# Optimization experiments

Hardware: AMD Instinct MI355X
Metric: run time of the kernel (lower is better)

## Reference

```python
import jax, jax.numpy as jnp
import numpy as np

B, L, C = 16, 2048, 128
FACTOR = 5
EPS = 1e-5


def setup_inputs() -> dict:
    key = jax.random.key(0)
    ks = jax.random.split(key, 16)
    U = min(FACTOR * int(np.ceil(np.log(L))), L)  # U_part == u == 40 for L=2048
    inp = {"x": jax.random.normal(ks[0], (B, L, C), jnp.float32)}
    scalar_names = ["Wq", "bq", "Wk", "bk", "Wv", "bv", "Wo", "bo", "w1", "b1", "w2", "b2"]
    for i, n in enumerate(scalar_names):
        inp[n] = jax.random.normal(ks[i + 1], (1,), jnp.float32) * 0.5
    inp["g1"] = jnp.ones((1,), jnp.float32)
    inp["beta1"] = jnp.zeros((1,), jnp.float32)
    inp["g2"] = jnp.ones((1,), jnp.float32)
    inp["beta2"] = jnp.zeros((1,), jnp.float32)
    # ProbAttention's random key-sampling indices (torch.randint(L_K, (L_Q, sample_k)))
    inp["index_sample"] = jax.random.randint(ks[14], (L, U), 0, L, dtype=jnp.int32)
    return inp


def _layernorm(x, g, b):
    # norm_dims=2 with d_model=1: normalize jointly over (seq_len, 1) == seq axis here
    m = x.mean(-1, keepdims=True)
    v = x.var(-1, keepdims=True)
    return (x - m) * jax.lax.rsqrt(v + EPS) * g + b


def reference(x, Wq, bq, Wk, bk, Wv, bv, Wo, bo, w1, b1, w2, b2,
              g1, beta1, g2, beta2, index_sample):
    U = index_sample.shape[1]  # sample_k == n_top (L_Q == L_K)
    batch_idx = jnp.arange(B)[:, None]

    def chan(xc):  # xc: [B, L] one channel, d_model=1 squeezed (H=1, D=1 -> scale=1)
        q = xc * Wq + bq
        k = xc * Wk + bk
        v = xc * Wv + bv
        # sparse measurement: sample U keys per query
        K_s = k[:, index_sample]                      # [B, L, U]
        QK = q[:, :, None] * K_s                      # [B, L, U]
        M = QK.max(-1) - QK.sum(-1) / L               # [B, L]
        _, M_top = jax.lax.top_k(M, U)                # [B, U] top-u query indices
        Qr = jnp.take_along_axis(q, M_top, axis=1)    # [B, U]
        scores = Qr[:, :, None] * k[:, None, :]       # [B, U, L], scale = 1/sqrt(1)
        attn = jax.nn.softmax(scores, axis=-1)
        upd = jnp.einsum('bul,bl->bu', attn, v)       # [B, U]
        # initial context = mean of V (mask_flag=False), updated at top queries
        ctx = jnp.broadcast_to(v.mean(1, keepdims=True), xc.shape)
        ctx = ctx.at[batch_idx, M_top].set(upd)       # [B, L]
        new_x = ctx * Wo + bo                          # out_projection
        x1 = _layernorm(xc + new_x, g1, beta1)
        y = jax.nn.gelu(x1 * w1 + b1, approximate=False)  # conv1 (1x1, 1->1) + gelu
        y = y * w2 + b2                                    # conv2 (1x1, 1->1)
        return _layernorm(x1 + y, g2, beta2)

    # all cfg.d_model encoder layers share one weight set -> vmap over channels
    return jax.vmap(chan, in_axes=2, out_axes=2)(x)  # [B, L, C]
```

## Files before the change

### kernel.cpp

```cpp
#include <hip/hip_runtime.h>
#include <math.h>

#define LL 2048
#define CC 128
#define BB 16
#define UU 40
#define NT 256
#define NW 4
#define EPSF 1e-5f

__device__ __forceinline__ float waveSum(float v) {
#pragma unroll
    for (int off = 1; off < 64; off <<= 1) v += __shfl_xor(v, off, 64);
    return v;
}
__device__ __forceinline__ float waveMax(float v) {
#pragma unroll
    for (int off = 1; off < 64; off <<= 1) v = fmaxf(v, __shfl_xor(v, off, 64));
    return v;
}
__device__ __forceinline__ float waveMin(float v) {
#pragma unroll
    for (int off = 1; off < 64; off <<= 1) v = fminf(v, __shfl_xor(v, off, 64));
    return v;
}
__device__ __forceinline__ float blockSum(float v, volatile float* scr) {
    v = waveSum(v);
    const int lane = threadIdx.x & 63, wid = threadIdx.x >> 6;
    __syncthreads();
    if (lane == 0) scr[wid] = v;
    __syncthreads();
    return scr[0] + scr[1] + scr[2] + scr[3];
}

__global__ __launch_bounds__(256) void transpose_dual(
    const float* __restrict__ x,  float* __restrict__ xT,
    const float* __restrict__ M,  float* __restrict__ MT) {
    __shared__ float t[32][33];
    const int z  = blockIdx.z;
    const int b  = (z < BB) ? z : (z - BB);
    const float* in  = (z < BB) ? x  : M;
    float* outp      = (z < BB) ? xT : MT;
    const int c0 = blockIdx.x * 32, l0 = blockIdx.y * 32;
    const int lx = threadIdx.x, ly = threadIdx.y;
    const float* base = in + ((size_t)b * LL + l0) * CC + c0;
#pragma unroll
    for (int i = 0; i < 4; ++i) t[ly + i * 8][lx] = base[(size_t)(ly + i * 8) * CC + lx];
    __syncthreads();
    float* obase = outp + ((size_t)b * CC + c0) * LL + l0;
#pragma unroll
    for (int i = 0; i < 4; ++i) obase[(size_t)(ly + i * 8) * LL + lx] = t[lx][ly + i * 8];
}
__global__ __launch_bounds__(256) void transpose_out(const float* __restrict__ in,
                                                     float* __restrict__ outp) {
    __shared__ float t[32][33];
    const int b  = blockIdx.z;
    const int l0 = blockIdx.x * 32, c0 = blockIdx.y * 32;
    const int lx = threadIdx.x, ly = threadIdx.y;
    const float* base = in + ((size_t)b * CC + c0) * LL + l0;
#pragma unroll
    for (int i = 0; i < 4; ++i) t[ly + i * 8][lx] = base[(size_t)(ly + i * 8) * LL + lx];
    __syncthreads();
    float* obase = outp + ((size_t)b * LL + l0) * CC + c0;
#pragma unroll
    for (int i = 0; i < 4; ++i) obase[(size_t)(ly + i * 8) * CC + lx] = t[lx][ly + i * 8];
}

__global__ __launch_bounds__(256) void agg_kernel(
    const float* __restrict__ x, const int* __restrict__ idx,
    const float* __restrict__ gWq, const float* __restrict__ gbq,
    const float* __restrict__ gWk, const float* __restrict__ gbk,
    float* __restrict__ M)
{
    __shared__ int s_idx[8 * UU];
    const int tid = threadIdx.x;
    const int g   = blockIdx.x;
    const int b   = ((g & 7) << 1) | ((g >> 3) & 1);
    const int l0  = (g >> 4) * 8;
    if (tid < 256)          s_idx[tid]       = idx[l0 * UU + tid];
    if (tid < 8 * UU - 256) s_idx[256 + tid] = idx[l0 * UU + 256 + tid];
    __syncthreads();

    const int s = tid & 31;
    const int r = tid >> 5;
    const int l = l0 + r;
    const float Wq = *gWq, bq = *gbq, Wk = *gWk, bk = *gbk;

    const float4* xb = (const float4*)(x + (size_t)b * LL * CC);
    float4 xo4 = xb[(size_t)l * 32 + s];
    float xo[4] = {xo4.x, xo4.y, xo4.z, xo4.w};

    float  mx[4] = {-3.4e38f, -3.4e38f, -3.4e38f, -3.4e38f};
    float  mn[4] = { 3.4e38f,  3.4e38f,  3.4e38f,  3.4e38f};
    double sm[4] = {0.0, 0.0, 0.0, 0.0};
    const int* rowp = &s_idx[r * UU];
#pragma unroll 8
    for (int u = 0; u < UU; ++u) {
        const int i = rowp[u];
        float4 xv = xb[(size_t)i * 32 + s];
        float xa[4] = {xv.x, xv.y, xv.z, xv.w};
#pragma unroll
        for (int t = 0; t < 4; ++t) {
            mx[t] = fmaxf(mx[t], xa[t]);
            mn[t] = fminf(mn[t], xa[t]);
            sm[t] += (double)xa[t];
        }
    }
    float mo[4];
#pragma unroll
    for (int t = 0; t < 4; ++t) {
        const float xH = (Wk >= 0.f) ? mx[t] : mn[t];
        const float xL = (Wk >= 0.f) ? mn[t] : mx[t];
        const float kH = __fadd_rn(__fmul_rn(xH, Wk), bk);
        const float kL = __fadd_rn(__fmul_rn(xL, Wk), bk);
        const float q  = __fadd_rn(__fmul_rn(xo[t], Wq), bq);
        const float t1 = __fmul_rn(q, (q >= 0.f) ? kH : kL);
        const double ks = (double)Wk * sm[t] + 40.0 * (double)bk;
        const float t2 = (float)(((double)q * ks) * (1.0 / 2048.0));
        mo[t] = __fsub_rn(t1, t2);
    }
    float4 Mo = make_float4(mo[0], mo[1], mo[2], mo[3]);
    ((float4*)(M + ((size_t)b * LL + l) * CC))[s] = Mo;
}

__global__ __launch_bounds__(NT) void informer_main(
    const float* __restrict__ xT,
    float* MoT,
    const float* __restrict__ gWq, const float* __restrict__ gbq,
    const float* __restrict__ gWk, const float* __restrict__ gbk,
    const float* __restrict__ gWv, const float* __restrict__ gbv,
    const float* __restrict__ gWo, const float* __restrict__ gbo,
    const float* __restrict__ gw1, const float* __restrict__ gb1,
    const float* __restrict__ gw2, const float* __restrict__ gb2,
    const float* __restrict__ gg1, const float* __restrict__ gbe1,
    const float* __restrict__ gg2, const float* __restrict__ gbe2)
{
    const int tid = threadIdx.x;
    const int ln  = tid & 63;
    const int wid = tid >> 6;
    const int blk = blockIdx.x;
    const int b   = blk >> 7;
    const int c   = blk & (CC - 1);

    __shared__ __align__(16) float s_xc[LL];
    __shared__ __align__(16) float s_wk[LL];
    __shared__ float s_red[NW];
    __shared__ float s_cv[NW * UU];
    __shared__ int   s_ci[NW * UU];
    __shared__ int   s_top[UU];
    __shared__ float s_upd[UU];

    const float Wq = *gWq, bq = *gbq, Wk = *gWk, bk = *gbk;
    const float Wv = *gWv, bv = *gbv, Wo = *gWo, bo = *gbo;
    const float w1 = *gw1, b1 = *gb1, w2 = *gw2, b2 = *gb2;
    const float g1 = *gg1, be1 = *gbe1, g2 = *gg2, be2 = *gbe2;

    const float4* xrow4 = (const float4*)(xT + ((size_t)b * CC + c) * LL);
    float* Mrow = MoT + ((size_t)b * CC + c) * LL;
    float4* orow4 = (float4*)Mrow;
    float4* s_xc4 = (float4*)s_xc;
    float4* s_wk4 = (float4*)s_wk;

    float4 kv[8], vv[8];
    float vsum = 0.f, kmn = 3.4e38f, kmx = -3.4e38f;
#pragma unroll
    for (int m = 0; m < 8; ++m) {
        float4 xv = xrow4[ln + m * 64];
        if (wid == 0) s_xc4[ln + m * 64] = xv;
        float4 kk, vx;
        kk.x = __fadd_rn(__fmul_rn(xv.x, Wk), bk);
        kk.y = __fadd_rn(__fmul_rn(xv.y, Wk), bk);
        kk.z = __fadd_rn(__fmul_rn(xv.z, Wk), bk);
        kk.w = __fadd_rn(__fmul_rn(xv.w, Wk), bk);
        vx.x = __fadd_rn(__fmul_rn(xv.x, Wv), bv);
        vx.y = __fadd_rn(__fmul_rn(xv.y, Wv), bv);
        vx.z = __fadd_rn(__fmul_rn(xv.z, Wv), bv);
        vx.w = __fadd_rn(__fmul_rn(xv.w, Wv), bv);
        kv[m] = kk; vv[m] = vx;
        vsum += vx.x + vx.y + vx.z + vx.w;
        kmx = fmaxf(kmx, fmaxf(fmaxf(kk.x, kk.y), fmaxf(kk.z, kk.w)));
        kmn = fminf(kmn, fminf(fminf(kk.x, kk.y), fminf(kk.z, kk.w)));
    }
    vsum = waveSum(vsum);
    kmx  = waveMax(kmx);
    kmn  = waveMin(kmn);
    const float vmean = vsum * (1.f / (float)LL);

    const int lbase = wid * 512 + ln;
    float mloc[8];
#pragma unroll
    for (int j = 0; j < 8; ++j) mloc[j] = Mrow[lbase + 64 * j];

    float wbv = mloc[0]; int wbi = lbase;
#pragma unroll
    for (int j = 1; j < 8; ++j)
        if (mloc[j] > wbv) { wbv = mloc[j]; wbi = lbase + 64 * j; }

    for (int t = 0; t < UU; ++t) {
        float rv = wbv; int ri = wbi;
#pragma unroll
        for (int off = 1; off < 64; off <<= 1) {
            float ov = __shfl_xor(rv, off, 64);
            int   oi = __shfl_xor(ri, off, 64);
            if (ov > rv || (ov == rv && oi < ri)) { rv = ov; ri = oi; }
        }
        if (ln == 0) { s_cv[wid * UU + t] = rv; s_ci[wid * UU + t] = ri; }
        if (wbi == ri) {
#pragma unroll
            for (int j = 0; j < 8; ++j) if (lbase + 64 * j == ri) mloc[j] = -3.4e38f;
            wbv = mloc[0]; wbi = lbase;
#pragma unroll
            for (int j = 1; j < 8; ++j)
                if (mloc[j] > wbv) { wbv = mloc[j]; wbi = lbase + 64 * j; }
        }
    }
    __syncthreads();

    if (wid == 0) {
        float c0v = s_cv[ln],      c1v = s_cv[ln + 64];
        int   c0i = s_ci[ln],      c1i = s_ci[ln + 64];
        float c2v = (ln < 32) ? s_cv[ln + 128] : -3.4e38f;
        int   c2i = (ln < 32) ? s_ci[ln + 128] : (LL + 1);
        for (int t = 0; t < UU; ++t) {
            float rv = c0v; int ri = c0i;
            if (c1v > rv || (c1v == rv && c1i < ri)) { rv = c1v; ri = c1i; }
            if (c2v > rv || (c2v == rv && c2i < ri)) { rv = c2v; ri = c2i; }
#pragma unroll
            for (int off = 1; off < 64; off <<= 1) {
                float ov = __shfl_xor(rv, off, 64);
                int   oi = __shfl_xor(ri, off, 64);
                if (ov > rv || (ov == rv && oi < ri)) { rv = ov; ri = oi; }
            }
            if (ln == 0) s_top[t] = ri;
            if (c0i == ri) c0v = -3.4e38f;
            else if (c1i == ri) c1v = -3.4e38f;
            else if (c2i == ri) c2v = -3.4e38f;
        }
    }
    __syncthreads();

    for (int r = 0; r < UU / NW; ++r) {
        const int u = r * NW + wid;
        const int p = s_top[u];
        const float qp = __fadd_rn(__fmul_rn(s_xc[p], Wq), bq);
        const float smax = (qp >= 0.f) ? __fmul_rn(qp, kmx) : __fmul_rn(qp, kmn);
        float se = 0.f, sev = 0.f;
#pragma unroll
        for (int m = 0; m < 8; ++m) {
            float4 kk = kv[m], vx = vv[m];
            float e0 = __expf(qp * kk.x - smax);
            float e1 = __expf(qp * kk.y - smax);
            float e2 = __expf(qp * kk.z - smax);
            float e3 = __expf(qp * kk.w - smax);
            se += e0 + e1 + e2 + e3;
            sev = fmaf(e0, vx.x, fmaf(e1, vx.y, fmaf(e2, vx.z, fmaf(e3, vx.w, sev))));
        }
        se  = waveSum(se);
        sev = waveSum(sev);
        if (ln == 0) s_upd[u] = sev / se;
    }
    __syncthreads();

#pragma unroll
    for (int m = 0; m < 2; ++m)
        s_wk4[tid + m * 256] = make_float4(vmean, vmean, vmean, vmean);
    __syncthreads();
    if (tid < UU) s_wk[s_top[tid]] = s_upd[tid];
    __syncthreads();

    float lsum = 0.f;
#pragma unroll
    for (int m = 0; m < 2; ++m) {
        const int f = tid + m * 256;
        float4 cx = s_wk4[f], xc = s_xc4[f], tv;
        tv.x = xc.x + __fadd_rn(__fmul_rn(cx.x, Wo), bo);
        tv.y = xc.y + __fadd_rn(__fmul_rn(cx.y, Wo), bo);
        tv.z = xc.z + __fadd_rn(__fmul_rn(cx.z, Wo), bo);
        tv.w = xc.w + __fadd_rn(__fmul_rn(cx.w, Wo), bo);
        s_wk4[f] = tv;
        lsum += tv.x + tv.y + tv.z + tv.w;
    }
    const float mean1 = blockSum(lsum, s_red) * (1.f / (float)LL);
    float lss = 0.f;
#pragma unroll
    for (int m = 0; m < 2; ++m) {
        float4 tv = s_wk4[tid + m * 256];
        float d0 = tv.x - mean1, d1 = tv.y - mean1, d2 = tv.z - mean1, d3 = tv.w - mean1;
        lss += d0 * d0 + d1 * d1 + d2 * d2 + d3 * d3;
    }
    const float var1 = blockSum(lss, s_red) * (1.f / (float)LL);
    const float rs1 = rsqrtf(var1 + EPSF);

    float lsum2 = 0.f;
#pragma unroll
    for (int m = 0; m < 2; ++m) {
        const int f = tid + m * 256;
        float4 tv = s_wk4[f], zz;
        {
            float x1 = (tv.x - mean1) * rs1 * g1 + be1;
            float a = x1 * w1 + b1;
            float y = 0.5f * a * (1.f + erff(a * 0.70710678118654752f));
            zz.x = x1 + (y * w2 + b2);
        }
        {
            float x1 = (tv.y - mean1) * rs1 * g1 + be1;
            float a = x1 * w1 + b1;
            float y = 0.5f * a * (1.f + erff(a * 0.70710678118654752f));
            zz.y = x1 + (y * w2 + b2);
        }
        {
            float x1 = (tv.z - mean1) * rs1 * g1 + be1;
            float a = x1 * w1 + b1;
            float y = 0.5f * a * (1.f + erff(a * 0.70710678118654752f));
            zz.z = x1 + (y * w2 + b2);
        }
        {
            float x1 = (tv.w - mean1) * rs1 * g1 + be1;
            float a = x1 * w1 + b1;
            float y = 0.5f * a * (1.f + erff(a * 0.70710678118654752f));
            zz.w = x1 + (y * w2 + b2);
        }
        s_wk4[f] = zz;
        lsum2 += zz.x + zz.y + zz.z + zz.w;
    }
    const float mean2 = blockSum(lsum2, s_red) * (1.f / (float)LL);
    float lss2 = 0.f;
#pragma unroll
    for (int m = 0; m < 2; ++m) {
        float4 zz = s_wk4[tid + m * 256];
        float d0 = zz.x - mean2, d1 = zz.y - mean2, d2 = zz.z - mean2, d3 = zz.w - mean2;
        lss2 += d0 * d0 + d1 * d1 + d2 * d2 + d3 * d3;
    }
    const float var2 = blockSum(lss2, s_red) * (1.f / (float)LL);
    const float rs2 = rsqrtf(var2 + EPSF);

#pragma unroll
    for (int m = 0; m < 2; ++m) {
        const int f = tid + m * 256;
        float4 zz = s_wk4[f], oo;
        oo.x = (zz.x - mean2) * rs2 * g2 + be2;
        oo.y = (zz.y - mean2) * rs2 * g2 + be2;
        oo.z = (zz.z - mean2) * rs2 * g2 + be2;
        oo.w = (zz.w - mean2) * rs2 * g2 + be2;
        orow4[f] = oo;
    }
}

__global__ __launch_bounds__(NT) void informer_fallback(
    const float* __restrict__ xin,
    const float* __restrict__ gWq, const float* __restrict__ gbq,
    const float* __restrict__ gWk, const float* __restrict__ gbk,
    const float* __restrict__ gWv, const float* __restrict__ gbv,
    const float* __restrict__ gWo, const float* __restrict__ gbo,
    const float* __restrict__ gw1, const float* __restrict__ gb1,
    const float* __restrict__ gw2, const float* __restrict__ gb2,
    const float* __restrict__ gg1, const float* __restrict__ gbe1,
    const float* __restrict__ gg2, const float* __restrict__ gbe2,
    const int* __restrict__ idx,
    float* __restrict__ outp)
{
    const int tid  = threadIdx.x;
    const int lane = tid & 63;
    const int wid  = tid >> 6;
    const int blk  = blockIdx.x;
    const int b    = blk >> 7;
    const int c    = blk & (CC - 1);

    __shared__ float  s_xc[LL];
    __shared__ float  s_kc[LL];
    __shared__ float  s_v[LL];
    __shared__ float  s_red[NW];
    __shared__ double s_cv[NW * UU];
    __shared__ int    s_ci[NW * UU];
    __shared__ int    s_top[UU];
    __shared__ float  s_upd[UU];

    const float Wq = *gWq, bq = *gbq, Wk = *gWk, bk = *gbk;
    const float Wv = *gWv, bv = *gbv, Wo = *gWo, bo = *gbo;
    const float w1 = *gw1, b1 = *gb1, w2 = *gw2, b2 = *gb2;
    const float g1 = *gg1, be1 = *gbe1, g2 = *gg2, be2 = *gbe2;

    const float* xrow = xin + (size_t)b * LL * CC + c;
    float* orow = outp + (size_t)b * LL * CC + c;

    float vsum = 0.f, kmn = 3.4e38f, kmx = -3.4e38f;
    for (int l = tid; l < LL; l += NT) {
        float xv = xrow[(size_t)l * CC];
        s_xc[l] = xv;
        float kvv = __fadd_rn(__fmul_rn(xv, Wk), bk);
        float vvv = __fadd_rn(__fmul_rn(xv, Wv), bv);
        s_kc[l] = kvv;
        s_v[l] = vvv;
        vsum += vvv;
        kmn = fminf(kmn, kvv);
        kmx = fmaxf(kmx, kvv);
    }
    const float vmean  = blockSum(vsum, s_red) * (1.f / (float)LL);
    float t1 = waveMax(kmx);
    __syncthreads();
    if (lane == 0) s_red[wid] = t1;
    __syncthreads();
    const float kmxAll = fmaxf(fmaxf(s_red[0], s_red[1]), fmaxf(s_red[2], s_red[3]));
    float t2 = waveMin(kmn);
    __syncthreads();
    if (lane == 0) s_red[wid] = t2;
    __syncthreads();
    const float kmnAll = fminf(fminf(s_red[0], s_red[1]), fminf(s_red[2], s_red[3]));

    double mloc[8];
#pragma unroll
    for (int j = 0; j < 8; ++j) {
        const int l = tid + NT * j;
        const float qv = __fadd_rn(__fmul_rn(s_xc[l], Wq), bq);
        const double qd = (double)qv;
        const int* row = idx + l * UU;
        float kmaxs = -3.4e38f, kmins = 3.4e38f;
        double ssum = 0.0;
#pragma unroll 8
        for (int u = 0; u < UU; ++u) {
            float kvv = s_kc[row[u]];
            kmaxs = fmaxf(kmaxs, kvv);
            kmins = fminf(kmins, kvv);
            ssum += (double)kvv;
        }
        double qmax = (qd >= 0.0) ? qd * (double)kmaxs : qd * (double)kmins;
        mloc[j] = qmax - qd * ssum * (1.0 / (double)LL);
    }

    double wbv = mloc[0]; int wbi = tid;
#pragma unroll
    for (int j = 1; j < 8; ++j)
        if (mloc[j] > wbv) { wbv = mloc[j]; wbi = tid + NT * j; }

    for (int t = 0; t < UU; ++t) {
        double rv = wbv; int ri = wbi;
#pragma unroll
        for (int off = 1; off < 64; off <<= 1) {
            double ov = __shfl_xor(rv, off, 64);
            int    oi = __shfl_xor(ri, off, 64);
            if (ov > rv || (ov == rv && oi < ri)) { rv = ov; ri = oi; }
        }
        if (lane == 0) { s_cv[wid * UU + t] = rv; s_ci[wid * UU + t] = ri; }
        if (wbi == ri) {
#pragma unroll
            for (int j = 0; j < 8; ++j) if ((tid + NT * j) == ri) mloc[j] = -1e300;
            wbv = mloc[0]; wbi = tid;
#pragma unroll
            for (int j = 1; j < 8; ++j)
                if (mloc[j] > wbv) { wbv = mloc[j]; wbi = tid + NT * j; }
        }
    }
    __syncthreads();

    if (wid == 0) {
        double c0v = s_cv[lane], c1v = s_cv[lane + 64];
        int    c0i = s_ci[lane], c1i = s_ci[lane + 64];
        double c2v = (lane < 32) ? s_cv[lane + 128] : -1e300;
        int    c2i = (lane < 32) ? s_ci[lane + 128] : (LL + 1);
        for (int t = 0; t < UU; ++t) {
            double rv = c0v; int ri = c0i;
            if (c1v > rv || (c1v == rv && c1i < ri)) { rv = c1v; ri = c1i; }
            if (c2v > rv || (c2v == rv && c2i < ri)) { rv = c2v; ri = c2i; }
#pragma unroll
            for (int off = 1; off < 64; off <<= 1) {
                double ov = __shfl_xor(rv, off, 64);
                int    oi = __shfl_xor(ri, off, 64);
                if (ov > rv || (ov == rv && oi < ri)) { rv = ov; ri = oi; }
            }
            if (lane == 0) s_top[t] = ri;
            if (c0i == ri) c0v = -1e300;
            else if (c1i == ri) c1v = -1e300;
            else if (c2i == ri) c2v = -1e300;
        }
    }
    __syncthreads();

    for (int r = 0; r < UU / NW; ++r) {
        const int u = r * NW + wid;
        const int p = s_top[u];
        const float qp = __fadd_rn(__fmul_rn(s_xc[p], Wq), bq);
        const float smax = (qp >= 0.f) ? qp * kmxAll : qp * kmnAll;
        float se = 0.f, sev = 0.f;
        for (int l = lane; l < LL; l += 64) {
            float e = __expf(qp * s_kc[l] - smax);
            se += e;
            sev = fmaf(e, s_v[l], sev);
        }
        se = waveSum(se); sev = waveSum(sev);
        if (lane == 0) s_upd[u] = sev / se;
    }
    __syncthreads();

    for (int l = tid; l < LL; l += NT) s_kc[l] = vmean;
    __syncthreads();
    if (tid < UU) s_kc[s_top[tid]] = s_upd[tid];
    __syncthreads();

    float lsum = 0.f;
    for (int l = tid; l < LL; l += NT) {
        float tv = s_xc[l] + __fadd_rn(__fmul_rn(s_kc[l], Wo), bo);
        s_kc[l] = tv;
        lsum += tv;
    }
    const float mean1 = blockSum(lsum, s_red) * (1.f / (float)LL);
    float lss = 0.f;
    for (int l = tid; l < LL; l += NT) { float d = s_kc[l] - mean1; lss += d * d; }
    const float var1 = blockSum(lss, s_red) * (1.f / (float)LL);
    const float rs1 = rsqrtf(var1 + EPSF);

    float lsum2 = 0.f;
    for (int l = tid; l < LL; l += NT) {
        float x1 = (s_kc[l] - mean1) * rs1 * g1 + be1;
        float a  = x1 * w1 + b1;
        float y  = 0.5f * a * (1.f + erff(a * 0.70710678118654752f));
        y = y * w2 + b2;
        float z = x1 + y;
        s_kc[l] = z;
        lsum2 += z;
    }
    const float mean2 = blockSum(lsum2, s_red) * (1.f / (float)LL);
    float lss2 = 0.f;
    for (int l = tid; l < LL; l += NT) { float d = s_kc[l] - mean2; lss2 += d * d; }
    const float var2 = blockSum(lss2, s_red) * (1.f / (float)LL);
    const float rs2 = rsqrtf(var2 + EPSF);

    for (int l = tid; l < LL; l += NT)
        orow[(size_t)l * CC] = (s_kc[l] - mean2) * rs2 * g2 + be2;
}

extern "C" void kernel_launch(void* const* d_in, const int* in_sizes, int n_in,
                              void* d_out, int out_size, void* d_ws, size_t ws_size,
                              hipStream_t stream) {
    const float* x   = (const float*)d_in[0];
    const float* Wq  = (const float*)d_in[1];
    const float* bq  = (const float*)d_in[2];
    const float* Wk  = (const float*)d_in[3];
    const float* bk  = (const float*)d_in[4];
    const float* Wv  = (const float*)d_in[5];
    const float* bv  = (const float*)d_in[6];
    const float* Wo  = (const float*)d_in[7];
    const float* bo  = (const float*)d_in[8];
    const float* w1  = (const float*)d_in[9];
    const float* b1  = (const float*)d_in[10];
    const float* w2  = (const float*)d_in[11];
    const float* b2  = (const float*)d_in[12];
    const float* g1  = (const float*)d_in[13];
    const float* be1 = (const float*)d_in[14];
    const float* g2  = (const float*)d_in[15];
    const float* be2 = (const float*)d_in[16];
    const int*   idx = (const int*)d_in[17];
    float* out = (float*)d_out;

    const size_t SZ = (size_t)BB * LL * CC * sizeof(float);

    if (ws_size >= 2 * SZ) {
        float* xT = (float*)d_ws;
        float* MT = (float*)((char*)d_ws + SZ);
        agg_kernel<<<dim3((LL / 8) * BB), dim3(256), 0, stream>>>(x, idx, Wq, bq, Wk, bk, out);
        transpose_dual<<<dim3(CC / 32, LL / 32, 2 * BB), dim3(32, 8), 0, stream>>>(x, xT, out, MT);
        informer_main<<<dim3(BB * CC), dim3(NT), 0, stream>>>(
            xT, MT, Wq, bq, Wk, bk, Wv, bv, Wo, bo, w1, b1, w2, b2,
            g1, be1, g2, be2);
        transpose_out<<<dim3(LL / 32, CC / 32, BB), dim3(32, 8), 0, stream>>>(MT, out);
    } else {
        informer_fallback<<<dim3(BB * CC), dim3(NT), 0, stream>>>(
            x, Wq, bq, Wk, bk, Wv, bv, Wo, bo, w1, b1, w2, b2,
            g1, be1, g2, be2, idx, out);
    }
}
```

Before: 292.8 us.

## Process one (batch,channel) row per wavefront instead of per block

The main kernel now gives each wavefront its own (b,c) row, with 4 rows per block, where before a whole 256-thread block handled one row. This removes the block-level syncthreads reductions and the two-stage cross-wave top-k merge, since top-40 selection, softmax updates and both layernorms now use only wave shuffles. The softmax pass handles 4 top queries at once and recomputes k from x in registers, and the k max/min come from the x max/min. In exchange each thread holds many more registers (8 float4 of M, x and temporaries), which may lower occupancy. The serial 40-step top-k loop is also now done by one wave over 2048 elements instead of being split across 4 waves.

```diff
diff --git a/kernel.cpp b/kernel.cpp
--- a/kernel.cpp
+++ b/kernel.cpp
@@ -31,6 +31,22 @@
     if (lane == 0) scr[wid] = v;
     __syncthreads();
     return scr[0] + scr[1] + scr[2] + scr[3];
+}
+__device__ __forceinline__ float blockMax(float v, volatile float* scr) {
+    v = waveMax(v);
+    const int lane = threadIdx.x & 63, wid = threadIdx.x >> 6;
+    __syncthreads();
+    if (lane == 0) scr[wid] = v;
+    __syncthreads();
+    return fmaxf(fmaxf(scr[0], scr[1]), fmaxf(scr[2], scr[3]));
+}
+__device__ __forceinline__ float blockMin(float v, volatile float* scr) {
+    v = waveMin(v);
+    const int lane = threadIdx.x & 63, wid = threadIdx.x >> 6;
+    __syncthreads();
+    if (lane == 0) scr[wid] = v;
+    __syncthreads();
+    return fminf(fminf(scr[0], scr[1]), fminf(scr[2], scr[3]));
 }
 
 __global__ __launch_bounds__(256) void transpose_dual(
@@ -123,7 +139,7 @@
     ((float4*)(M + ((size_t)b * LL + l) * CC))[s] = Mo;
 }
 
-__global__ __launch_bounds__(NT) void informer_main(
+__global__ __launch_bounds__(NT) void rowBC(
     const float* __restrict__ xT,
     float* MoT,
     const float* __restrict__ gWq, const float* __restrict__ gbq,
@@ -138,164 +154,152 @@
     const int tid = threadIdx.x;
     const int ln  = tid & 63;
     const int wid = tid >> 6;
-    const int blk = blockIdx.x;
-    const int b   = blk >> 7;
-    const int c   = blk & (CC - 1);
-
-    __shared__ __align__(16) float s_xc[LL];
-    __shared__ __align__(16) float s_wk[LL];
-    __shared__ float s_red[NW];
-    __shared__ float s_cv[NW * UU];
-    __shared__ int   s_ci[NW * UU];
-    __shared__ int   s_top[UU];
-    __shared__ float s_upd[UU];
+    const int r   = blockIdx.x * 4 + wid;
+
+    __shared__ __align__(16) float s_ctx[4][LL];
+    __shared__ int s_top[4][UU];
 
     const float Wq = *gWq, bq = *gbq, Wk = *gWk, bk = *gbk;
     const float Wv = *gWv, bv = *gbv, Wo = *gWo, bo = *gbo;
     const float w1 = *gw1, b1 = *gb1, w2 = *gw2, b2 = *gb2;
     const float g1 = *gg1, be1 = *gbe1, g2 = *gg2, be2 = *gbe2;
 
-    const float4* xrow4 = (const float4*)(xT + ((size_t)b * CC + c) * LL);
-    float* Mrow = MoT + ((size_t)b * CC + c) * LL;
+    const float*  xrow  = xT + (size_t)r * LL;
+    const float4* xrow4 = (const float4*)xrow;
+    float* Mrow = MoT + (size_t)r * LL;
+    const float4* mrow4 = (const float4*)Mrow;
     float4* orow4 = (float4*)Mrow;
-    float4* s_xc4 = (float4*)s_xc;
-    float4* s_wk4 = (float4*)s_wk;
-
-    float4 kv[8], vv[8];
-    float vsum = 0.f, kmn = 3.4e38f, kmx = -3.4e38f;
-#pragma unroll
-    for (int m = 0; m < 8; ++m) {
-        float4 xv = xrow4[ln + m * 64];
-        if (wid == 0) s_xc4[ln + m * 64] = xv;
-        float4 kk, vx;
-        kk.x = __fadd_rn(__fmul_rn(xv.x, Wk), bk);
-        kk.y = __fadd_rn(__fmul_rn(xv.y, Wk), bk);
-        kk.z = __fadd_rn(__fmul_rn(xv.z, Wk), bk);
-        kk.w = __fadd_rn(__fmul_rn(xv.w, Wk), bk);
-        vx.x = __fadd_rn(__fmul_rn(xv.x, Wv), bv);
-        vx.y = __fadd_rn(__fmul_rn(xv.y, Wv), bv);
-        vx.z = __fadd_rn(__fmul_rn(xv.z, Wv), bv);
-        vx.w = __fadd_rn(__fmul_rn(xv.w, Wv), bv);
-        kv[m] = kk; vv[m] = vx;
-        vsum += vx.x + vx.y + vx.z + vx.w;
-        kmx = fmaxf(kmx, fmaxf(fmaxf(kk.x, kk.y), fmaxf(kk.z, kk.w)));
-        kmn = fminf(kmn, fminf(fminf(kk.x, kk.y), fminf(kk.z, kk.w)));
-    }
-    vsum = waveSum(vsum);
-    kmx  = waveMax(kmx);
-    kmn  = waveMin(kmn);
-    const float vmean = vsum * (1.f / (float)LL);
-
-    const int lbase = wid * 512 + ln;
-    float mloc[8];
-#pragma unroll
-    for (int j = 0; j < 8; ++j) mloc[j] = Mrow[lbase + 64 * j];
-
-    float wbv = mloc[0]; int wbi = lbase;
-#pragma unroll
-    for (int j = 1; j < 8; ++j)
-        if (mloc[j] > wbv) { wbv = mloc[j]; wbi = lbase + 64 * j; }
-
+    float4* lds4  = (float4*)s_ctx[wid];
+
+    float4 mv[8];
+#pragma unroll
+    for (int m = 0; m < 8; ++m) mv[m] = mrow4[ln + m * 64];
+
+    float bvv = -3.4e38f; int bii = LL + 1;
+#pragma unroll
+    for (int m = 0; m < 8; ++m) {
+        const int l0 = 4 * (ln + 64 * m);
+        if (mv[m].x > bvv) { bvv = mv[m].x; bii = l0; }
+        if (mv[m].y > bvv) { bvv = mv[m].y; bii = l0 + 1; }
+        if (mv[m].z > bvv) { bvv = mv[m].z; bii = l0 + 2; }
+        if (mv[m].w > bvv) { bvv = mv[m].w; bii = l0 + 3; }
+    }
     for (int t = 0; t < UU; ++t) {
-        float rv = wbv; int ri = wbi;
+        float rv = bvv; int ri = bii;
 #pragma unroll
         for (int off = 1; off < 64; off <<= 1) {
             float ov = __shfl_xor(rv, off, 64);
             int   oi = __shfl_xor(ri, off, 64);
             if (ov > rv || (ov == rv && oi < ri)) { rv = ov; ri = oi; }
         }
-        if (ln == 0) { s_cv[wid * UU + t] = rv; s_ci[wid * UU + t] = ri; }
-        if (wbi == ri) {
-#pragma unroll
-            for (int j = 0; j < 8; ++j) if (lbase + 64 * j == ri) mloc[j] = -3.4e38f;
-            wbv = mloc[0]; wbi = lbase;
-#pragma unroll
-            for (int j = 1; j < 8; ++j)
-                if (mloc[j] > wbv) { wbv = mloc[j]; wbi = lbase + 64 * j; }
-        }
-    }
-    __syncthreads();
-
-    if (wid == 0) {
-        float c0v = s_cv[ln],      c1v = s_cv[ln + 64];
-        int   c0i = s_ci[ln],      c1i = s_ci[ln + 64];
-        float c2v = (ln < 32) ? s_cv[ln + 128] : -3.4e38f;
-        int   c2i = (ln < 32) ? s_ci[ln + 128] : (LL + 1);
-        for (int t = 0; t < UU; ++t) {
-            float rv = c0v; int ri = c0i;
-            if (c1v > rv || (c1v == rv && c1i < ri)) { rv = c1v; ri = c1i; }
-            if (c2v > rv || (c2v == rv && c2i < ri)) { rv = c2v; ri = c2i; }
-#pragma unroll
-            for (int off = 1; off < 64; off <<= 1) {
-                float ov = __shfl_xor(rv, off, 64);
-                int   oi = __shfl_xor(ri, off, 64);
-                if (ov > rv || (ov == rv && oi < ri)) { rv = ov; ri = oi; }
+        if (ln == 0) s_top[wid][t] = ri;
+        if (bii == ri) {
+#pragma unroll
+            for (int m = 0; m < 8; ++m) {
+                const int l0 = 4 * (ln + 64 * m);
+                if (l0     == ri) mv[m].x = -3.4e38f;
+                if (l0 + 1 == ri) mv[m].y = -3.4e38f;
+                if (l0 + 2 == ri) mv[m].z = -3.4e38f;
+                if (l0 + 3 == ri) mv[m].w = -3.4e38f;
             }
-            if (ln == 0) s_top[t] = ri;
-            if (c0i == ri) c0v = -3.4e38f;
-            else if (c1i == ri) c1v = -3.4e38f;
-            else if (c2i == ri) c2v = -3.4e38f;
-        }
-    }
-    __syncthreads();
-
-    for (int r = 0; r < UU / NW; ++r) {
-        const int u = r * NW + wid;
-        const int p = s_top[u];
-        const float qp = __fadd_rn(__fmul_rn(s_xc[p], Wq), bq);
-        const float smax = (qp >= 0.f) ? __fmul_rn(qp, kmx) : __fmul_rn(qp, kmn);
-        float se = 0.f, sev = 0.f;
+            bvv = -3.4e38f; bii = LL + 1;
+#pragma unroll
+            for (int m = 0; m < 8; ++m) {
+                const int l0 = 4 * (ln + 64 * m);
+                if (mv[m].x > bvv) { bvv = mv[m].x; bii = l0; }
+                if (mv[m].y > bvv) { bvv = mv[m].y; bii = l0 + 1; }
+                if (mv[m].z > bvv) { bvv = mv[m].z; bii = l0 + 2; }
+                if (mv[m].w > bvv) { bvv = mv[m].w; bii = l0 + 3; }
+            }
+        }
+    }
+
+    float4 xc[8];
+    float vsum = 0.f, xmx = -3.4e38f, xmn = 3.4e38f;
+#pragma unroll
+    for (int m = 0; m < 8; ++m) {
+        float4 xv = xrow4[ln + m * 64];
+        xc[m] = xv;
+        vsum += __fadd_rn(__fmul_rn(xv.x, Wv), bv) + __fadd_rn(__fmul_rn(xv.y, Wv), bv)
+              + __fadd_rn(__fmul_rn(xv.z, Wv), bv) + __fadd_rn(__fmul_rn(xv.w, Wv), bv);
+        xmx = fmaxf(xmx, fmaxf(fmaxf(xv.x, xv.y), fmaxf(xv.z, xv.w)));
+        xmn = fminf(xmn, fminf(fminf(xv.x, xv.y), fminf(xv.z, xv.w)));
+    }
+    vsum = waveSum(vsum);
+    xmx  = waveMax(xmx);
+    xmn  = waveMin(xmn);
+    const float vmean = vsum * (1.f / (float)LL);
+    const float kmx = __fadd_rn(__fmul_rn((Wk >= 0.f) ? xmx : xmn, Wk), bk);
+    const float kmn = __fadd_rn(__fmul_rn((Wk >= 0.f) ? xmn : xmx, Wk), bk);
+
+#pragma unroll
+    for (int m = 0; m < 8; ++m)
+        lds4[ln + m * 64] = make_float4(vmean, vmean, vmean, vmean);
+
+    for (int g = 0; g < UU / 4; ++g) {
+        int p[4]; float qp[4], sm[4];
+#pragma unroll
+        for (int q = 0; q < 4; ++q) {
+            p[q] = s_top[wid][g * 4 + q];
+            const float xq = xrow[p[q]];
+            qp[q] = __fadd_rn(__fmul_rn(xq, Wq), bq);
+            sm[q] = (qp[q] >= 0.f) ? __fmul_rn(qp[q], kmx) : __fmul_rn(qp[q], kmn);
+        }
+        float se[4] = {0.f, 0.f, 0.f, 0.f};
+        float sx[4] = {0.f, 0.f, 0.f, 0.f};
 #pragma unroll
         for (int m = 0; m < 8; ++m) {
-            float4 kk = kv[m], vx = vv[m];
-            float e0 = __expf(qp * kk.x - smax);
-            float e1 = __expf(qp * kk.y - smax);
-            float e2 = __expf(qp * kk.z - smax);
-            float e3 = __expf(qp * kk.w - smax);
-            se += e0 + e1 + e2 + e3;
-            sev = fmaf(e0, vx.x, fmaf(e1, vx.y, fmaf(e2, vx.z, fmaf(e3, vx.w, sev))));
-        }
-        se  = waveSum(se);
-        sev = waveSum(sev);
-        if (ln == 0) s_upd[u] = sev / se;
-    }
-    __syncthreads();
-
-#pragma unroll
-    for (int m = 0; m < 2; ++m)
-        s_wk4[tid + m * 256] = make_float4(vmean, vmean, vmean, vmean);
-    __syncthreads();
-    if (tid < UU) s_wk[s_top[tid]] = s_upd[tid];
-    __syncthreads();
-
+            float4 x4 = xc[m];
+            float4 k4;
+            k4.x = __fadd_rn(__fmul_rn(x4.x, Wk), bk);
+            k4.y = __fadd_rn(__fmul_rn(x4.y, Wk), bk);
+            k4.z = __fadd_rn(__fmul_rn(x4.z, Wk), bk);
+            k4.w = __fadd_rn(__fmul_rn(x4.w, Wk), bk);
+#pragma unroll
+            for (int q = 0; q < 4; ++q) {
+                float e;
+                e = __expf(fmaf(qp[q], k4.x, -sm[q])); se[q] += e; sx[q] = fmaf(e, x4.x, sx[q]);
+                e = __expf(fmaf(qp[q], k4.y, -sm[q])); se[q] += e; sx[q] = fmaf(e, x4.y, sx[q]);
+                e = __expf(fmaf(qp[q], k4.z, -sm[q])); se[q] += e; sx[q] = fmaf(e, x4.z, sx[q]);
+                e = __expf(fmaf(qp[q], k4.w, -sm[q])); se[q] += e; sx[q] = fmaf(e, x4.w, sx[q]);
+            }
+        }
+#pragma unroll
+        for (int q = 0; q < 4; ++q) {
+            const float seA = waveSum(se[q]);
+            const float sxA = waveSum(sx[q]);
+            const float upd = (Wv * sxA + bv * seA) / seA;
+            if (ln == 0) s_ctx[wid][p[q]] = upd;
+        }
+    }
+
+    float4 tt[8];
     float lsum = 0.f;
 #pragma unroll
-    for (int m = 0; m < 2; ++m) {
-        const int f = tid + m * 256;
-        float4 cx = s_wk4[f], xc = s_xc4[f], tv;
-        tv.x = xc.x + __fadd_rn(__fmul_rn(cx.x, Wo), bo);
-        tv.y = xc.y + __fadd_rn(__fmul_rn(cx.y, Wo), bo);
-        tv.z = xc.z + __fadd_rn(__fmul_rn(cx.z, Wo), bo);
-        tv.w = xc.w + __fadd_rn(__fmul_rn(cx.w, Wo), bo);
-        s_wk4[f] = tv;
+    for (int m = 0; m < 8; ++m) {
+        float4 cx = lds4[ln + m * 64], xv = xc[m], tv;
+        tv.x = xv.x + __fadd_rn(__fmul_rn(cx.x, Wo), bo);
+        tv.y = xv.y + __fadd_rn(__fmul_rn(cx.y, Wo), bo);
+        tv.z = xv.z + __fadd_rn(__fmul_rn(cx.z, Wo), bo);
+        tv.w = xv.w + __fadd_rn(__fmul_rn(cx.w, Wo), bo);
+        tt[m] = tv;
         lsum += tv.x + tv.y + tv.z + tv.w;
     }
-    const float mean1 = blockSum(lsum, s_red) * (1.f / (float)LL);
+    const float mean1 = waveSum(lsum) * (1.f / (float)LL);
     float lss = 0.f;
 #pragma unroll
-    for (int m = 0; m < 2; ++m) {
-        float4 tv = s_wk4[tid + m * 256];
+    for (int m = 0; m < 8; ++m) {
+        float4 tv = tt[m];
         float d0 = tv.x - mean1, d1 = tv.y - mean1, d2 = tv.z - mean1, d3 = tv.w - mean1;
         lss += d0 * d0 + d1 * d1 + d2 * d2 + d3 * d3;
     }
-    const float var1 = blockSum(lss, s_red) * (1.f / (float)LL);
+    const float var1 = waveSum(lss) * (1.f / (float)LL);
     const float rs1 = rsqrtf(var1 + EPSF);
 
     float lsum2 = 0.f;
 #pragma unroll
-    for (int m = 0; m < 2; ++m) {
-        const int f = tid + m * 256;
-        float4 tv = s_wk4[f], zz;
+    for (int m = 0; m < 8; ++m) {
+        float4 tv = tt[m], zz;
         {
             float x1 = (tv.x - mean1) * rs1 * g1 + be1;
             float a = x1 * w1 + b1;
@@ -320,29 +324,28 @@
             float y = 0.5f * a * (1.f + erff(a * 0.70710678118654752f));
             zz.w = x1 + (y * w2 + b2);
         }
-        s_wk4[f] = zz;
+        tt[m] = zz;
         lsum2 += zz.x + zz.y + zz.z + zz.w;
     }
-    const float mean2 = blockSum(lsum2, s_red) * (1.f / (float)LL);
+    const float mean2 = waveSum(lsum2) * (1.f / (float)LL);
     float lss2 = 0.f;
 #pragma unroll
-    for (int m = 0; m < 2; ++m) {
-        float4 zz = s_wk4[tid + m * 256];
+    for (int m = 0; m < 8; ++m) {
+        float4 zz = tt[m];
         float d0 = zz.x - mean2, d1 = zz.y - mean2, d2 = zz.z - mean2, d3 = zz.w - mean2;
         lss2 += d0 * d0 + d1 * d1 + d2 * d2 + d3 * d3;
     }
-    const float var2 = blockSum(lss2, s_red) * (1.f / (float)LL);
+    const float var2 = waveSum(lss2) * (1.f / (float)LL);
     const float rs2 = rsqrtf(var2 + EPSF);
 
 #pragma unroll
-    for (int m = 0; m < 2; ++m) {
-        const int f = tid + m * 256;
-        float4 zz = s_wk4[f], oo;
+    for (int m = 0; m < 8; ++m) {
+        float4 zz = tt[m], oo;
         oo.x = (zz.x - mean2) * rs2 * g2 + be2;
         oo.y = (zz.y - mean2) * rs2 * g2 + be2;
         oo.z = (zz.z - mean2) * rs2 * g2 + be2;
         oo.w = (zz.w - mean2) * rs2 * g2 + be2;
-        orow4[f] = oo;
+        orow4[ln + m * 64] = oo;
     }
 }
 
@@ -396,16 +399,8 @@
         kmx = fmaxf(kmx, kvv);
     }
     const float vmean  = blockSum(vsum, s_red) * (1.f / (float)LL);
-    float t1 = waveMax(kmx);
-    __syncthreads();
-    if (lane == 0) s_red[wid] = t1;
-    __syncthreads();
-    const float kmxAll = fmaxf(fmaxf(s_red[0], s_red[1]), fmaxf(s_red[2], s_red[3]));
-    float t2 = waveMin(kmn);
-    __syncthreads();
-    if (lane == 0) s_red[wid] = t2;
-    __syncthreads();
-    const float kmnAll = fminf(fminf(s_red[0], s_red[1]), fminf(s_red[2], s_red[3]));
+    const float kmxAll = blockMax(kmx, s_red);
+    const float kmnAll = blockMin(kmn, s_red);
 
     double mloc[8];
 #pragma unroll
@@ -558,7 +553,7 @@
         float* MT = (float*)((char*)d_ws + SZ);
         agg_kernel<<<dim3((LL / 8) * BB), dim3(256), 0, stream>>>(x, idx, Wq, bq, Wk, bk, out);
         transpose_dual<<<dim3(CC / 32, LL / 32, 2 * BB), dim3(32, 8), 0, stream>>>(x, xT, out, MT);
-        informer_main<<<dim3(BB * CC), dim3(NT), 0, stream>>>(
+        rowBC<<<dim3(BB * CC / 4), dim3(NT), 0, stream>>>(
             xT, MT, Wq, bq, Wk, bk, Wv, bv, Wo, bo, w1, b1, w2, b2,
             g1, be1, g2, be2);
         transpose_out<<<dim3(LL / 32, CC / 32, BB), dim3(32, 8), 0, stream>>>(MT, out);
```

Result: faster. 235.0 us (-19.7%).
